# Optimization experiments

Hardware: AMD Instinct MI355X
Metric: run time of the kernel (lower is better)

## Reference

```python
import jax, jax.numpy as jnp
import numpy as np

FEATURE_DIM = 1024
N_CONCEPTS = 32768
BATCH = 1024
TEMPERATURE = 0.1
EPS = 1e-12  # matches torch F.normalize eps


def l2_normalize(x, axis=-1):
    n = jnp.linalg.norm(x, axis=axis, keepdims=True)
    return x / jnp.maximum(n, EPS)


def setup_inputs() -> dict:
    key = jax.random.key(0)
    k1, k2, k3, k4 = jax.random.split(key, 4)
    features = jax.random.normal(k1, (BATCH, FEATURE_DIM), dtype=jnp.float32)
    # Linear projection params (original inits to identity/zeros; random exercises the math)
    W = jnp.eye(FEATURE_DIM, dtype=jnp.float32) + 0.02 * jax.random.normal(k2, (FEATURE_DIM, FEATURE_DIM), dtype=jnp.float32)
    b = 0.01 * jax.random.normal(k3, (FEATURE_DIM,), dtype=jnp.float32)
    prototypes = l2_normalize(jax.random.normal(k4, (N_CONCEPTS, FEATURE_DIM), dtype=jnp.float32))
    return {"features": features, "W": W, "b": b, "prototypes": prototypes}


def reference(features, W, b, prototypes):
    # projection: features @ W.T + b   (torch nn.Linear convention)
    projected = jnp.einsum('bd,ed->be', features, W) + b          # [B, D]
    projected = l2_normalize(projected)                           # [B, D]
    # cosine similarity against all prototypes
    similarities = jnp.einsum('bd,kd->bk', projected, prototypes) # [B, K]
    activations = jax.nn.softmax(similarities / TEMPERATURE, axis=-1)
    best_idx = jnp.argmax(similarities, axis=-1)                  # [B] int
    return activations, best_idx
```

## Files before the change

kernel.cpp:

```cpp
#include <hip/hip_runtime.h>
#include <hip/hip_bf16.h>


typedef __attribute__((ext_vector_type(8))) short short8;
typedef __attribute__((ext_vector_type(4))) float floatx4;

__device__ __forceinline__ unsigned short f2bf(float f) {
  unsigned int u = __float_as_uint(f);
  u += 0x7fffu + ((u >> 16) & 1u);
  return (unsigned short)(u >> 16);
}
__device__ __forceinline__ float bf2f(unsigned short h) {
  return __uint_as_float(((unsigned int)h) << 16);
}

__global__ __launch_bounds__(256) void prep_convert(
    const float* __restrict__ protos, unsigned short* __restrict__ protoB,
    const float* __restrict__ features, unsigned short* __restrict__ Fh,
    unsigned short* __restrict__ Fm, unsigned short* __restrict__ Fl,
    const float* __restrict__ W, unsigned short* __restrict__ Wh,
    unsigned short* __restrict__ Wm, unsigned short* __restrict__ Wl) {
  const int blk = blockIdx.x;
  if (blk < 16384) {
    int i = blk * 256 + threadIdx.x;
    const float4* s4 = (const float4*)protos;
    float4 a = s4[2 * i];
    float4 b = s4[2 * i + 1];
    short8 o;
    o[0] = (short)f2bf(a.x); o[1] = (short)f2bf(a.y);
    o[2] = (short)f2bf(a.z); o[3] = (short)f2bf(a.w);
    o[4] = (short)f2bf(b.x); o[5] = (short)f2bf(b.y);
    o[6] = (short)f2bf(b.z); o[7] = (short)f2bf(b.w);
    ((short8*)protoB)[i] = o;
    return;
  }
  const float* src; unsigned short *H, *Md, *L; int i;
  if (blk < 17408) {
    src = features; H = Fh; Md = Fm; L = Fl;
    i = (blk - 16384) * 256 + threadIdx.x;
  } else {
    src = W; H = Wh; Md = Wm; L = Wl;
    i = (blk - 17408) * 256 + threadIdx.x;
  }
  float4 x = ((const float4*)src)[i];
  ushort4 h, m, l;
  float v, r;
  v = x.x; h.x = f2bf(v); r = v - bf2f(h.x); m.x = f2bf(r); l.x = f2bf(r - bf2f(m.x));
  v = x.y; h.y = f2bf(v); r = v - bf2f(h.y); m.y = f2bf(r); l.y = f2bf(r - bf2f(m.y));
  v = x.z; h.z = f2bf(v); r = v - bf2f(h.z); m.z = f2bf(r); l.z = f2bf(r - bf2f(m.z));
  v = x.w; h.w = f2bf(v); r = v - bf2f(h.w); m.w = f2bf(r); l.w = f2bf(r - bf2f(m.w));
  ((ushort4*)H)[i] = h; ((ushort4*)Md)[i] = m; ((ushort4*)L)[i] = l;
}


#define BARRIER() asm volatile("s_barrier" ::: "memory")
#define WAITLGKM()                                        \
  do {                                                    \
    asm volatile("s_waitcnt lgkmcnt(0)" ::: "memory");    \
    __builtin_amdgcn_sched_barrier(0);                    \
  } while (0)
#define WAITVM4() asm volatile("s_waitcnt vmcnt(4)" ::: "memory")

#define STAGE(OP, SLOT, H, KT)                                                 \
  do {                                                                         \
    const unsigned short* _s0 = (OP ? pB0 : pA0) + (H)*131072 + (KT)*64;       \
    const unsigned short* _s1 = (OP ? pB1 : pA1) + (H)*131072 + (KT)*64;       \
    __builtin_amdgcn_global_load_lds(                                          \
        (const __attribute__((address_space(1))) void*)_s0,                    \
        (__attribute__((address_space(3))) void*)(&lds[SLOT][OP][(H)*8192 + w * 512]), \
        16, 0, 0);                                                             \
    __builtin_amdgcn_global_load_lds(                                          \
        (const __attribute__((address_space(1))) void*)_s1,                    \
        (__attribute__((address_space(3))) void*)(&lds[SLOT][OP][(H)*8192 + 4096 + w * 512]), \
        16, 0, 0);                                                             \
  } while (0)

#define READ4(dst, base, off, rowadd)                                          \
  _Pragma("unroll") for (int q = 0; q < 4; q++)                                \
      dst[q] = *(const short8*)((base) + (off) + ((rowadd) + q) * 2048);

#define MFMA16(AB, BB, MBASE)                                                  \
  do {                                                                         \
    __builtin_amdgcn_sched_barrier(0);                                         \
    __builtin_amdgcn_s_setprio(1);                                             \
    _Pragma("unroll") for (int mf = 0; mf < 4; mf++)                           \
        _Pragma("unroll") for (int nf = 0; nf < 4; nf++)                       \
            acc[(MBASE) + mf][nf] = __builtin_amdgcn_mfma_f32_16x16x32_bf16(   \
                AB[mf], BB[nf], acc[(MBASE) + mf][nf], 0, 0, 0);               \
    __builtin_amdgcn_s_setprio(0);                                             \
    __builtin_amdgcn_sched_barrier(0);                                         \
  } while (0)

__global__ __launch_bounds__(512, 2) void gemm_nt_bf16_256(
    const unsigned short* __restrict__ A, const unsigned short* __restrict__ B,
    float* __restrict__ C, float* __restrict__ ml, int M, int N, int K) {
  __shared__ unsigned short lds[2][2][16384];
  const int tid = threadIdx.x;
  const int w = tid >> 6, lane = tid & 63;
  const int wr = w >> 2, wc = w & 3;
  const int fr = lane & 15, koff8 = lane >> 4;

  const int bid = blockIdx.x;
  const int c8 = bid & 7, u = bid >> 3;
  const int nb = c8 * 16 + (u >> 2);
  const long tn = (long)nb * 256;
  const long tm = (long)(u & 3) * 256;

  const int idx0 = w * 64 + lane;
  const int idx1 = 512 + idx0;
  const int rh0 = idx0 >> 3, sc0 = (idx0 & 7) ^ (rh0 & 7);
  const int rh1 = idx1 >> 3, sc1 = (idx1 & 7) ^ (rh1 & 7);
  const unsigned short* pA0 = A + (tm + rh0) * 1024 + sc0 * 8;
  const unsigned short* pA1 = A + (tm + rh1) * 1024 + sc1 * 8;
  const unsigned short* pB0 = B + (tn + rh0) * 1024 + sc0 * 8;
  const unsigned short* pB1 = B + (tn + rh1) * 1024 + sc1 * 8;

  const int rA = wr * 128 + fr;
  const int rB = wc * 64 + fr;
  const int offA0 = rA * 128 + ((koff8 ^ (rA & 7)) << 4);
  const int offA1 = rA * 128 + (((koff8 ^ 4) ^ (rA & 7)) << 4);
  const int offB0 = rB * 128 + ((koff8 ^ (rB & 7)) << 4);
  const int offB1 = rB * 128 + (((koff8 ^ 4) ^ (rB & 7)) << 4);

  const char* ldsc = (const char*)&lds[0][0][0];
#define LDSA(s) (ldsc + (s)*65536)
#define LDSB(s) (ldsc + (s)*65536 + 32768)

  floatx4 acc[8][4];
#pragma unroll
  for (int i = 0; i < 8; i++)
#pragma unroll
    for (int j = 0; j < 4; j++) acc[i][j] = (floatx4){0.f, 0.f, 0.f, 0.f};

  short8 a0[4], a1[4], a2[4], b0[4], b1[4];

  STAGE(0, 0, 0, 0); STAGE(0, 0, 1, 0); STAGE(1, 0, 0, 0); STAGE(1, 0, 1, 0);
  STAGE(0, 1, 0, 1); STAGE(0, 1, 1, 1);
  WAITVM4();
  BARRIER();

#pragma unroll 1
  for (int i = 0; i < 8; i++) {
    const int t1 = 2 * i + 1;
    const int t2 = (2 * i + 2) & 15;
    const int t3 = (2 * i + 3) & 15;

    READ4(a0, LDSA(0), offA0, 0);
    READ4(a1, LDSA(0), offA0, 4);
    READ4(b0, LDSB(0), offB0, 0);
    STAGE(1, 1, 0, t1);
    BARRIER(); WAITLGKM();
    MFMA16(a0, b0, 0);
    BARRIER();
    READ4(a0, LDSA(0), offA1, 0);
    READ4(a2, LDSA(0), offA1, 4);
    READ4(b1, LDSB(0), offB1, 0);
    STAGE(1, 1, 1, t1);
    BARRIER(); WAITLGKM();
    MFMA16(a1, b0, 4);
    BARRIER();
    STAGE(0, 0, 0, t2);
    BARRIER();
    MFMA16(a0, b1, 0);
    BARRIER();
    STAGE(0, 0, 1, t2);
    WAITVM4();
    BARRIER();
    MFMA16(a2, b1, 4);
    BARRIER();

    READ4(a0, LDSA(1), offA0, 0);
    READ4(a1, LDSA(1), offA0, 4);
    READ4(b0, LDSB(1), offB0, 0);
    STAGE(1, 0, 0, t2);
    BARRIER(); WAITLGKM();
    MFMA16(a0, b0, 0);
    BARRIER();
    READ4(a0, LDSA(1), offA1, 0);
    READ4(a2, LDSA(1), offA1, 4);
    READ4(b1, LDSB(1), offB1, 0);
    STAGE(1, 0, 1, t2);
    BARRIER(); WAITLGKM();
    MFMA16(a1, b0, 4);
    BARRIER();
    STAGE(0, 1, 0, t3);
    BARRIER();
    MFMA16(a0, b1, 0);
    BARRIER();
    STAGE(0, 1, 1, t3);
    WAITVM4();
    BARRIER();
    MFMA16(a2, b1, 4);
    BARRIER();
  }

  {
    float2* mlx = (float2*)&lds[0][0][0];
    const int hi = lane >> 4;
#pragma unroll
    for (int mf = 0; mf < 8; mf++)
#pragma unroll
      for (int r = 0; r < 4; r++) {
        float z0 = acc[mf][0][r] * 10.f, z1 = acc[mf][1][r] * 10.f;
        float z2 = acc[mf][2][r] * 10.f, z3 = acc[mf][3][r] * 10.f;
        float mz = fmaxf(fmaxf(z0, z1), fmaxf(z2, z3));
#pragma unroll
        for (int off = 1; off < 16; off <<= 1) mz = fmaxf(mz, __shfl_xor(mz, off));
        float ls = __expf(z0 - mz) + __expf(z1 - mz) +
                   __expf(z2 - mz) + __expf(z3 - mz);
#pragma unroll
        for (int off = 1; off < 16; off <<= 1) ls += __shfl_xor(ls, off);
        if (fr == 0) mlx[(wr * 128 + mf * 16 + hi * 4 + r) * 4 + wc] =
            make_float2(mz, ls);
      }
    __syncthreads();
    if (tid < 256) {
      const int wrr = tid >> 7, row = tid & 127;
      float2 q0 = mlx[(wrr * 128 + row) * 4 + 0];
      float2 q1 = mlx[(wrr * 128 + row) * 4 + 1];
      float2 q2 = mlx[(wrr * 128 + row) * 4 + 2];
      float2 q3 = mlx[(wrr * 128 + row) * 4 + 3];
      float Mb = fmaxf(fmaxf(q0.x, q1.x), fmaxf(q2.x, q3.x));
      float Lb = q0.y * __expf(q0.x - Mb) + q1.y * __expf(q1.x - Mb) +
                 q2.y * __expf(q2.x - Mb) + q3.y * __expf(q3.x - Mb);
      ((float2*)ml)[(long)nb * 1024 + (tm + wrr * 128 + row)] =
          make_float2(Mb, Lb);
    }
  }

  const long crow = tm + wr * 128 + ((lane >> 4) * 4);
  const long ccol = tn + wc * 64 + fr;
#pragma unroll
  for (int mf = 0; mf < 8; mf++)
#pragma unroll
    for (int nf = 0; nf < 4; nf++)
#pragma unroll
      for (int r = 0; r < 4; r++)
        C[(crow + mf * 16 + r) * (long)N + ccol + nf * 16] = acc[mf][nf][r];
#undef LDSA
#undef LDSB
}

__global__ __launch_bounds__(256) void gemm_split6_nt(
    const unsigned short* __restrict__ Ah, const unsigned short* __restrict__ Am,
    const unsigned short* __restrict__ Al, const unsigned short* __restrict__ Bh,
    const unsigned short* __restrict__ Bm, const unsigned short* __restrict__ Bl,
    float* __restrict__ Cpart, int M, int N, int K) {
  __shared__ unsigned short sA[3][64 * 32];
  __shared__ unsigned short sB[3][64 * 32];
  const int tid  = threadIdx.x;
  const int wave = tid >> 6;
  const int lane = tid & 63;
  const long tm = (long)blockIdx.y * 64;
  const long tn = (long)blockIdx.x * 64;
  const int wm = (wave & 1) * 32;
  const int wn = (wave >> 1) * 32;
  const int ksize = K / gridDim.z;
  const int kbase = blockIdx.z * ksize;
  float* C = Cpart + (size_t)blockIdx.z * M * N;

  floatx4 accH[2][2], accL[2][2];
#pragma unroll
  for (int i = 0; i < 2; i++)
#pragma unroll
    for (int j = 0; j < 2; j++) {
      accH[i][j] = (floatx4){0.f, 0.f, 0.f, 0.f};
      accL[i][j] = (floatx4){0.f, 0.f, 0.f, 0.f};
    }

  const int rstage = tid >> 2;
  const int cstage = (tid & 3) * 8;
  const long aoff = (tm + rstage) * (long)K + cstage;
  const long boff = (tn + rstage) * (long)K + cstage;
  const unsigned short* Asrc[3] = {Ah + aoff, Am + aoff, Al + aoff};
  const unsigned short* Bsrc[3] = {Bh + boff, Bm + boff, Bl + boff};

  for (int k0 = kbase; k0 < kbase + ksize; k0 += 32) {
#pragma unroll
    for (int p = 0; p < 3; p++) {
      __builtin_amdgcn_global_load_lds(
          (const __attribute__((address_space(1))) void*)(Asrc[p] + k0),
          (__attribute__((address_space(3))) void*)(sA[p] + wave * 512), 16, 0, 0);
      __builtin_amdgcn_global_load_lds(
          (const __attribute__((address_space(1))) void*)(Bsrc[p] + k0),
          (__attribute__((address_space(3))) void*)(sB[p] + wave * 512), 16, 0, 0);
    }
    __syncthreads();

    const int fr = lane & 15;
    const int koff = (lane >> 4) * 8;
    short8 a_[3][2], b_[3][2];
#pragma unroll
    for (int p = 0; p < 3; p++)
#pragma unroll
      for (int mf = 0; mf < 2; mf++) {
        a_[p][mf] = *(const short8*)(sA[p] + (wm + mf * 16 + fr) * 32 + koff);
        b_[p][mf] = *(const short8*)(sB[p] + (wn + mf * 16 + fr) * 32 + koff);
      }
#pragma unroll
    for (int mf = 0; mf < 2; mf++)
#pragma unroll
      for (int nf = 0; nf < 2; nf++) {
        accH[mf][nf] = __builtin_amdgcn_mfma_f32_16x16x32_bf16(
            a_[0][mf], b_[0][nf], accH[mf][nf], 0, 0, 0);
        accL[mf][nf] = __builtin_amdgcn_mfma_f32_16x16x32_bf16(
            a_[0][mf], b_[1][nf], accL[mf][nf], 0, 0, 0);
        accL[mf][nf] = __builtin_amdgcn_mfma_f32_16x16x32_bf16(
            a_[1][mf], b_[0][nf], accL[mf][nf], 0, 0, 0);
        accL[mf][nf] = __builtin_amdgcn_mfma_f32_16x16x32_bf16(
            a_[0][mf], b_[2][nf], accL[mf][nf], 0, 0, 0);
        accL[mf][nf] = __builtin_amdgcn_mfma_f32_16x16x32_bf16(
            a_[2][mf], b_[0][nf], accL[mf][nf], 0, 0, 0);
        accL[mf][nf] = __builtin_amdgcn_mfma_f32_16x16x32_bf16(
            a_[1][mf], b_[1][nf], accL[mf][nf], 0, 0, 0);
      }
    __syncthreads();
  }

  const long crow = tm + wm + ((lane >> 4) * 4);
  const long ccol = tn + wn + (lane & 15);
#pragma unroll
  for (int mf = 0; mf < 2; mf++)
#pragma unroll
    for (int nf = 0; nf < 2; nf++)
#pragma unroll
      for (int r = 0; r < 4; r++)
        C[(crow + mf * 16 + r) * (long)N + ccol + nf * 16] =
            accH[mf][nf][r] + accL[mf][nf][r];
}

__global__ __launch_bounds__(256) void norm_bias_rows(
    const float* __restrict__ P0, const float* __restrict__ P1, int nparts,
    const float* __restrict__ bias, unsigned short* __restrict__ Pn,
    float* __restrict__ Pn32) {
  const int b = blockIdx.x, tid = threadIdx.x;
  float4 v = ((const float4*)(P0 + (long)b * 1024))[tid];
  if (nparts == 2) {
    float4 v1 = ((const float4*)(P1 + (long)b * 1024))[tid];
    v.x += v1.x; v.y += v1.y; v.z += v1.z; v.w += v1.w;
  }
  float4 bb = ((const float4*)bias)[tid];
  v.x += bb.x; v.y += bb.y; v.z += bb.z; v.w += bb.w;
  float ss = v.x * v.x + v.y * v.y + v.z * v.z + v.w * v.w;
#pragma unroll
  for (int off = 32; off > 0; off >>= 1) ss += __shfl_down(ss, off);
  __shared__ float wred[4];
  if ((tid & 63) == 0) wred[tid >> 6] = ss;
  __syncthreads();
  float tot = wred[0] + wred[1] + wred[2] + wred[3];
  float inv = 1.0f / fmaxf(sqrtf(tot), 1e-12f);
  float4 p = make_float4(v.x * inv, v.y * inv, v.z * inv, v.w * inv);
  ((float4*)Pn32)[b * 256 + tid] = p;
  ushort4 o;
  o.x = f2bf(p.x); o.y = f2bf(p.y); o.z = f2bf(p.z); o.w = f2bf(p.w);
  ((ushort4*)Pn)[b * 256 + tid] = o;
}

__global__ __launch_bounds__(256) void softmax_argmax_refine(
    float* __restrict__ S, const float* __restrict__ Pn32,
    const float* __restrict__ protos, const float* __restrict__ ml,
    float* __restrict__ idx_out) {
  const int b = blockIdx.x, tid = threadIdx.x;
  const int wave = tid >> 6, lane = tid & 63;
  float4* row4 = (float4*)(S + (long)b * 32768);

  __shared__ float2 mlred[2];
  __shared__ int cand[64];
  __shared__ int ncand;
  if (tid == 0) ncand = 0;

  if (wave < 2) {
    float2 p = ((const float2*)ml)[(long)tid * 1024 + b];
    float m = p.x, l = p.y;
#pragma unroll
    for (int off = 1; off < 64; off <<= 1) {
      float mo = __shfl_xor(m, off);
      float lo = __shfl_xor(l, off);
      float nm = fmaxf(m, mo);
      l = l * __expf(m - nm) + lo * __expf(mo - nm);
      m = nm;
    }
    if (lane == 0) mlred[wave] = make_float2(m, l);
  }
  __syncthreads();
  const float m0 = mlred[0].x, m1 = mlred[1].x;
  const float Mz = fmaxf(m0, m1);
  const float L = mlred[0].y * __expf(m0 - Mz) + mlred[1].y * __expf(m1 - Mz);
  const float invL = 1.0f / L;
  const float thr = Mz * 0.1f - 0.012f;

#pragma unroll 4
  for (int it = 0; it < 32; it++) {
    int i4 = tid + 256 * it;
    float4 v = row4[i4];
    if (fmaxf(fmaxf(v.x, v.y), fmaxf(v.z, v.w)) >= thr) {
      if (v.x >= thr) { int p = atomicAdd(&ncand, 1); if (p < 64) cand[p] = i4 * 4; }
      if (v.y >= thr) { int p = atomicAdd(&ncand, 1); if (p < 64) cand[p] = i4 * 4 + 1; }
      if (v.z >= thr) { int p = atomicAdd(&ncand, 1); if (p < 64) cand[p] = i4 * 4 + 2; }
      if (v.w >= thr) { int p = atomicAdd(&ncand, 1); if (p < 64) cand[p] = i4 * 4 + 3; }
    }
    float4 e;
    e.x = __expf(v.x * 10.f - Mz) * invL;
    e.y = __expf(v.y * 10.f - Mz) * invL;
    e.z = __expf(v.z * 10.f - Mz) * invL;
    e.w = __expf(v.w * 10.f - Mz) * invL;
    row4[i4] = e;
  }
  __syncthreads();
  int n = ncand < 64 ? ncand : 64;

  float4 pv = ((const float4*)(Pn32 + (long)b * 1024))[tid];
  __shared__ double dred[4];
  double best = -1e300;
  int besti = 0x7fffffff;
  for (int c = 0; c < n; c++) {
    int k = cand[c];
    float4 kv = ((const float4*)(protos + (long)k * 1024))[tid];
    double d = (double)pv.x * kv.x + (double)pv.y * kv.y +
               (double)pv.z * kv.z + (double)pv.w * kv.w;
#pragma unroll
    for (int off = 32; off > 0; off >>= 1) d += __shfl_down(d, off);
    if (lane == 0) dred[wave] = d;
    __syncthreads();
    if (tid == 0) {
      double tot = dred[0] + dred[1] + dred[2] + dred[3];
      if (tot > best || (tot == best && k < besti)) { best = tot; besti = k; }
    }
    __syncthreads();
  }
  if (tid == 0) idx_out[b] = (float)besti;
}

extern "C" void kernel_launch(void* const* d_in, const int* in_sizes, int n_in,
                              void* d_out, int out_size, void* d_ws, size_t ws_size,
                              hipStream_t stream) {
  const float* features = (const float*)d_in[0];
  const float* W        = (const float*)d_in[1];
  const float* bias     = (const float*)d_in[2];
  const float* protos   = (const float*)d_in[3];

  const size_t MB = 1024 * 1024;
  char* ws = (char*)d_ws;
  unsigned short* protoB = (unsigned short*)ws;
  unsigned short* Fh = (unsigned short*)(ws + 64 * MB);
  unsigned short* Fm = (unsigned short*)(ws + 66 * MB);
  unsigned short* Fl = (unsigned short*)(ws + 68 * MB);
  unsigned short* Wh = (unsigned short*)(ws + 70 * MB);
  unsigned short* Wm = (unsigned short*)(ws + 72 * MB);
  unsigned short* Wl = (unsigned short*)(ws + 74 * MB);
  float*          P0 = (float*)(ws + 76 * MB);
  float*          P1 = (float*)(ws + 80 * MB);
  unsigned short* Pn   = (unsigned short*)(ws + 64 * MB);
  float*          Pn32 = (float*)(ws + 66 * MB);
  float*          mlb  = (float*)(ws + 76 * MB);

  const int ksplit = (ws_size >= 84 * MB) ? 2 : 1;

  float* S = (float*)d_out;
  float* idx_out = S + (size_t)1024 * 32768;

  prep_convert<<<18432, 256, 0, stream>>>(protos, protoB, features, Fh, Fm, Fl,
                                          W, Wh, Wm, Wl);
  gemm_split6_nt<<<dim3(16, 16, ksplit), 256, 0, stream>>>(
      Fh, Fm, Fl, Wh, Wm, Wl, P0, 1024, 1024, 1024);
  norm_bias_rows<<<1024, 256, 0, stream>>>(P0, P1, ksplit, bias, Pn, Pn32);
  gemm_nt_bf16_256<<<512, 512, 0, stream>>>(Pn, protoB, S, mlb, 1024, 32768, 1024);
  softmax_argmax_refine<<<1024, 256, 0, stream>>>(S, Pn32, protos, mlb, idx_out);
}
```

Before: 410.3 us.

## Store similarity logits as bf16 and compute softmax stats in a separate pass

The big GEMM now writes its similarity matrix as bf16 into the upper half of each output row instead of fp32, and no longer computes per-tile max/sum in its epilogue. The softmax kernel stages each bf16 row into LDS, runs an online max/sum reduction there, then writes the fp32 probabilities in place and collects argmax candidates using a slightly wider threshold. This roughly halves the GEMM's store traffic and drops the second fp32 read of the matrix, at the cost of bf16 rounding in the softmax inputs and 64KB of LDS per softmax block. The projection GEMM split-K also goes from 2 to 4, with the extra partials placed in the output buffer.

```diff
diff --git a/kernel.cpp b/kernel.cpp
--- a/kernel.cpp
+++ b/kernel.cpp
@@ -93,7 +93,7 @@
 
 __global__ __launch_bounds__(512, 2) void gemm_nt_bf16_256(
     const unsigned short* __restrict__ A, const unsigned short* __restrict__ B,
-    float* __restrict__ C, float* __restrict__ ml, int M, int N, int K) {
+    unsigned short* __restrict__ Cb, int M, int N, int K) {
   __shared__ unsigned short lds[2][2][16384];
   const int tid = threadIdx.x;
   const int w = tid >> 6, lane = tid & 63;
@@ -194,49 +194,17 @@
     BARRIER();
   }
 
-  {
-    float2* mlx = (float2*)&lds[0][0][0];
-    const int hi = lane >> 4;
-#pragma unroll
-    for (int mf = 0; mf < 8; mf++)
-#pragma unroll
-      for (int r = 0; r < 4; r++) {
-        float z0 = acc[mf][0][r] * 10.f, z1 = acc[mf][1][r] * 10.f;
-        float z2 = acc[mf][2][r] * 10.f, z3 = acc[mf][3][r] * 10.f;
-        float mz = fmaxf(fmaxf(z0, z1), fmaxf(z2, z3));
-#pragma unroll
-        for (int off = 1; off < 16; off <<= 1) mz = fmaxf(mz, __shfl_xor(mz, off));
-        float ls = __expf(z0 - mz) + __expf(z1 - mz) +
-                   __expf(z2 - mz) + __expf(z3 - mz);
-#pragma unroll
-        for (int off = 1; off < 16; off <<= 1) ls += __shfl_xor(ls, off);
-        if (fr == 0) mlx[(wr * 128 + mf * 16 + hi * 4 + r) * 4 + wc] =
-            make_float2(mz, ls);
-      }
-    __syncthreads();
-    if (tid < 256) {
-      const int wrr = tid >> 7, row = tid & 127;
-      float2 q0 = mlx[(wrr * 128 + row) * 4 + 0];
-      float2 q1 = mlx[(wrr * 128 + row) * 4 + 1];
-      float2 q2 = mlx[(wrr * 128 + row) * 4 + 2];
-      float2 q3 = mlx[(wrr * 128 + row) * 4 + 3];
-      float Mb = fmaxf(fmaxf(q0.x, q1.x), fmaxf(q2.x, q3.x));
-      float Lb = q0.y * __expf(q0.x - Mb) + q1.y * __expf(q1.x - Mb) +
-                 q2.y * __expf(q2.x - Mb) + q3.y * __expf(q3.x - Mb);
-      ((float2*)ml)[(long)nb * 1024 + (tm + wrr * 128 + row)] =
-          make_float2(Mb, Lb);
-    }
-  }
-
   const long crow = tm + wr * 128 + ((lane >> 4) * 4);
   const long ccol = tn + wc * 64 + fr;
+  const long rs2 = 2 * (long)N;
 #pragma unroll
   for (int mf = 0; mf < 8; mf++)
 #pragma unroll
     for (int nf = 0; nf < 4; nf++)
 #pragma unroll
       for (int r = 0; r < 4; r++)
-        C[(crow + mf * 16 + r) * (long)N + ccol + nf * 16] = acc[mf][nf][r];
+        Cb[(crow + mf * 16 + r) * rs2 + N + ccol + nf * 16] =
+            f2bf(acc[mf][nf][r]);
 #undef LDSA
 #undef LDSB
 }
@@ -245,7 +213,7 @@
     const unsigned short* __restrict__ Ah, const unsigned short* __restrict__ Am,
     const unsigned short* __restrict__ Al, const unsigned short* __restrict__ Bh,
     const unsigned short* __restrict__ Bm, const unsigned short* __restrict__ Bl,
-    float* __restrict__ Cpart, int M, int N, int K) {
+    float* __restrict__ Cpart, float* __restrict__ Cpart2, int M, int N, int K) {
   __shared__ unsigned short sA[3][64 * 32];
   __shared__ unsigned short sB[3][64 * 32];
   const int tid  = threadIdx.x;
@@ -257,7 +225,8 @@
   const int wn = (wave >> 1) * 32;
   const int ksize = K / gridDim.z;
   const int kbase = blockIdx.z * ksize;
-  float* C = Cpart + (size_t)blockIdx.z * M * N;
+  float* C = (blockIdx.z < 2) ? (Cpart + (size_t)blockIdx.z * M * N)
+                              : (Cpart2 + (size_t)(blockIdx.z - 2) * M * N);
 
   floatx4 accH[2][2], accL[2][2];
 #pragma unroll
@@ -330,14 +299,18 @@
 }
 
 __global__ __launch_bounds__(256) void norm_bias_rows(
-    const float* __restrict__ P0, const float* __restrict__ P1, int nparts,
+    const float* __restrict__ P0, const float* __restrict__ P1,
+    const float* __restrict__ P2, const float* __restrict__ P3, int nparts,
     const float* __restrict__ bias, unsigned short* __restrict__ Pn,
     float* __restrict__ Pn32) {
   const int b = blockIdx.x, tid = threadIdx.x;
   float4 v = ((const float4*)(P0 + (long)b * 1024))[tid];
-  if (nparts == 2) {
+  if (nparts == 4) {
     float4 v1 = ((const float4*)(P1 + (long)b * 1024))[tid];
-    v.x += v1.x; v.y += v1.y; v.z += v1.z; v.w += v1.w;
+    float4 v2 = ((const float4*)(P2 + (long)b * 1024))[tid];
+    float4 v3 = ((const float4*)(P3 + (long)b * 1024))[tid];
+    v.x += v1.x + v2.x + v3.x; v.y += v1.y + v2.y + v3.y;
+    v.z += v1.z + v2.z + v3.z; v.w += v1.w + v2.w + v3.w;
   }
   float4 bb = ((const float4*)bias)[tid];
   v.x += bb.x; v.y += bb.y; v.z += bb.z; v.w += bb.w;
@@ -356,55 +329,97 @@
   ((ushort4*)Pn)[b * 256 + tid] = o;
 }
 
-__global__ __launch_bounds__(256) void softmax_argmax_refine(
-    float* __restrict__ S, const float* __restrict__ Pn32,
-    const float* __restrict__ protos, const float* __restrict__ ml,
-    float* __restrict__ idx_out) {
+__global__ __launch_bounds__(256) void softmax_argmax_bf16(
+    float* __restrict__ out, const float* __restrict__ Pn32,
+    const float* __restrict__ protos, float* __restrict__ idx_out) {
   const int b = blockIdx.x, tid = threadIdx.x;
   const int wave = tid >> 6, lane = tid & 63;
-  float4* row4 = (float4*)(S + (long)b * 32768);
-
-  __shared__ float2 mlred[2];
+  __shared__ unsigned short srw[32768];
+  __shared__ float sm_[4], sl_[4];
   __shared__ int cand[64];
   __shared__ int ncand;
+
+  const float4* src4 =
+      (const float4*)((const char*)out + (size_t)b * 131072 + 65536);
+  float4* lds4 = (float4*)srw;
+#pragma unroll
+  for (int j = 0; j < 16; j++) lds4[tid + 256 * j] = src4[tid + 256 * j];
   if (tid == 0) ncand = 0;
-
-  if (wave < 2) {
-    float2 p = ((const float2*)ml)[(long)tid * 1024 + b];
-    float m = p.x, l = p.y;
-#pragma unroll
-    for (int off = 1; off < 64; off <<= 1) {
-      float mo = __shfl_xor(m, off);
-      float lo = __shfl_xor(l, off);
-      float nm = fmaxf(m, mo);
-      l = l * __expf(m - nm) + lo * __expf(mo - nm);
-      m = nm;
+  __syncthreads();
+
+  float m = -3.4e38f, l = 0.f;
+#pragma unroll 4
+  for (int j = 0; j < 16; j++) {
+    short8 v = ((const short8*)srw)[tid + 256 * j];
+    float z0 = bf2f((unsigned short)v[0]) * 10.f;
+    float z1 = bf2f((unsigned short)v[1]) * 10.f;
+    float z2 = bf2f((unsigned short)v[2]) * 10.f;
+    float z3 = bf2f((unsigned short)v[3]) * 10.f;
+    float z4 = bf2f((unsigned short)v[4]) * 10.f;
+    float z5 = bf2f((unsigned short)v[5]) * 10.f;
+    float z6 = bf2f((unsigned short)v[6]) * 10.f;
+    float z7 = bf2f((unsigned short)v[7]) * 10.f;
+    float m8 = fmaxf(fmaxf(fmaxf(z0, z1), fmaxf(z2, z3)),
+                     fmaxf(fmaxf(z4, z5), fmaxf(z6, z7)));
+    float nm = fmaxf(m, m8);
+    float s = __expf(z0 - nm) + __expf(z1 - nm) + __expf(z2 - nm) +
+              __expf(z3 - nm) + __expf(z4 - nm) + __expf(z5 - nm) +
+              __expf(z6 - nm) + __expf(z7 - nm);
+    l = l * __expf(m - nm) + s;
+    m = nm;
+  }
+#pragma unroll
+  for (int off = 1; off < 64; off <<= 1) {
+    float mo = __shfl_xor(m, off);
+    float lo = __shfl_xor(l, off);
+    float nm = fmaxf(m, mo);
+    l = l * __expf(m - nm) + lo * __expf(mo - nm);
+    m = nm;
+  }
+  if (lane == 0) { sm_[wave] = m; sl_[wave] = l; }
+  __syncthreads();
+  const float Mz = fmaxf(fmaxf(sm_[0], sm_[1]), fmaxf(sm_[2], sm_[3]));
+  const float L = sl_[0] * __expf(sm_[0] - Mz) + sl_[1] * __expf(sm_[1] - Mz) +
+                  sl_[2] * __expf(sm_[2] - Mz) + sl_[3] * __expf(sm_[3] - Mz);
+  const float invL = 1.0f / L;
+  const float thr = Mz * 0.1f - 0.016f;
+
+  float* orow = out + (long)b * 32768;
+#pragma unroll 2
+  for (int j = 0; j < 16; j++) {
+    const int i8 = tid + 256 * j;
+    short8 v = ((const short8*)srw)[i8];
+    float s0 = bf2f((unsigned short)v[0]);
+    float s1 = bf2f((unsigned short)v[1]);
+    float s2 = bf2f((unsigned short)v[2]);
+    float s3 = bf2f((unsigned short)v[3]);
+    float s4 = bf2f((unsigned short)v[4]);
+    float s5 = bf2f((unsigned short)v[5]);
+    float s6 = bf2f((unsigned short)v[6]);
+    float s7 = bf2f((unsigned short)v[7]);
+    float mx = fmaxf(fmaxf(fmaxf(s0, s1), fmaxf(s2, s3)),
+                     fmaxf(fmaxf(s4, s5), fmaxf(s6, s7)));
+    if (mx >= thr) {
+      if (s0 >= thr) { int p = atomicAdd(&ncand, 1); if (p < 64) cand[p] = i8 * 8 + 0; }
+      if (s1 >= thr) { int p = atomicAdd(&ncand, 1); if (p < 64) cand[p] = i8 * 8 + 1; }
+      if (s2 >= thr) { int p = atomicAdd(&ncand, 1); if (p < 64) cand[p] = i8 * 8 + 2; }
+      if (s3 >= thr) { int p = atomicAdd(&ncand, 1); if (p < 64) cand[p] = i8 * 8 + 3; }
+      if (s4 >= thr) { int p = atomicAdd(&ncand, 1); if (p < 64) cand[p] = i8 * 8 + 4; }
+      if (s5 >= thr) { int p = atomicAdd(&ncand, 1); if (p < 64) cand[p] = i8 * 8 + 5; }
+      if (s6 >= thr) { int p = atomicAdd(&ncand, 1); if (p < 64) cand[p] = i8 * 8 + 6; }
+      if (s7 >= thr) { int p = atomicAdd(&ncand, 1); if (p < 64) cand[p] = i8 * 8 + 7; }
     }
-    if (lane == 0) mlred[wave] = make_float2(m, l);
-  }
-  __syncthreads();
-  const float m0 = mlred[0].x, m1 = mlred[1].x;
-  const float Mz = fmaxf(m0, m1);
-  const float L = mlred[0].y * __expf(m0 - Mz) + mlred[1].y * __expf(m1 - Mz);
-  const float invL = 1.0f / L;
-  const float thr = Mz * 0.1f - 0.012f;
-
-#pragma unroll 4
-  for (int it = 0; it < 32; it++) {
-    int i4 = tid + 256 * it;
-    float4 v = row4[i4];
-    if (fmaxf(fmaxf(v.x, v.y), fmaxf(v.z, v.w)) >= thr) {
-      if (v.x >= thr) { int p = atomicAdd(&ncand, 1); if (p < 64) cand[p] = i4 * 4; }
-      if (v.y >= thr) { int p = atomicAdd(&ncand, 1); if (p < 64) cand[p] = i4 * 4 + 1; }
-      if (v.z >= thr) { int p = atomicAdd(&ncand, 1); if (p < 64) cand[p] = i4 * 4 + 2; }
-      if (v.w >= thr) { int p = atomicAdd(&ncand, 1); if (p < 64) cand[p] = i4 * 4 + 3; }
-    }
-    float4 e;
-    e.x = __expf(v.x * 10.f - Mz) * invL;
-    e.y = __expf(v.y * 10.f - Mz) * invL;
-    e.z = __expf(v.z * 10.f - Mz) * invL;
-    e.w = __expf(v.w * 10.f - Mz) * invL;
-    row4[i4] = e;
+    float4 e0, e1;
+    e0.x = __expf(s0 * 10.f - Mz) * invL;
+    e0.y = __expf(s1 * 10.f - Mz) * invL;
+    e0.z = __expf(s2 * 10.f - Mz) * invL;
+    e0.w = __expf(s3 * 10.f - Mz) * invL;
+    e1.x = __expf(s4 * 10.f - Mz) * invL;
+    e1.y = __expf(s5 * 10.f - Mz) * invL;
+    e1.z = __expf(s6 * 10.f - Mz) * invL;
+    e1.w = __expf(s7 * 10.f - Mz) * invL;
+    ((float4*)orow)[2 * i8] = e0;
+    ((float4*)orow)[2 * i8 + 1] = e1;
   }
   __syncthreads();
   int n = ncand < 64 ? ncand : 64;
@@ -450,11 +465,12 @@
   unsigned short* Wl = (unsigned short*)(ws + 74 * MB);
   float*          P0 = (float*)(ws + 76 * MB);
   float*          P1 = (float*)(ws + 80 * MB);
+  float*          P2 = (float*)d_out;
+  float*          P3 = (float*)((char*)d_out + 4 * MB);
   unsigned short* Pn   = (unsigned short*)(ws + 64 * MB);
   float*          Pn32 = (float*)(ws + 66 * MB);
-  float*          mlb  = (float*)(ws + 76 * MB);
-
-  const int ksplit = (ws_size >= 84 * MB) ? 2 : 1;
+
+  const int ksplit = (ws_size >= 84 * MB) ? 4 : 1;
 
   float* S = (float*)d_out;
   float* idx_out = S + (size_t)1024 * 32768;
@@ -462,8 +478,10 @@
   prep_convert<<<18432, 256, 0, stream>>>(protos, protoB, features, Fh, Fm, Fl,
                                           W, Wh, Wm, Wl);
   gemm_split6_nt<<<dim3(16, 16, ksplit), 256, 0, stream>>>(
-      Fh, Fm, Fl, Wh, Wm, Wl, P0, 1024, 1024, 1024);
-  norm_bias_rows<<<1024, 256, 0, stream>>>(P0, P1, ksplit, bias, Pn, Pn32);
-  gemm_nt_bf16_256<<<512, 512, 0, stream>>>(Pn, protoB, S, mlb, 1024, 32768, 1024);
-  softmax_argmax_refine<<<1024, 256, 0, stream>>>(S, Pn32, protos, mlb, idx_out);
-}
+      Fh, Fm, Fl, Wh, Wm, Wl, P0, P2, 1024, 1024, 1024);
+  norm_bias_rows<<<1024, 256, 0, stream>>>(P0, P1, P2, P3, ksplit, bias, Pn,
+                                           Pn32);
+  gemm_nt_bf16_256<<<512, 512, 0, stream>>>(Pn, protoB, (unsigned short*)d_out,
+                                            1024, 32768, 1024);
+  softmax_argmax_bf16<<<1024, 256, 0, stream>>>(S, Pn32, protos, idx_out);
+}
```

New measurement: 400.2 us. 2.5% less time.
